# Performance work log

Hardware: AMD Instinct MI355X
Metric: run time of the kernel (lower is better)

## Reference

```python
import jax, jax.numpy as jnp
import numpy as np

B, T, D, H, V = 4096, 193, 50, 50, 11


def setup_inputs() -> dict:
    key = jax.random.key(0)
    ks = jax.random.split(key, 7)
    s = 1.0 / np.sqrt(H)
    return {
        "x": jax.random.normal(ks[0], (B, T, D), dtype=jnp.float32),
        "W_ih": jax.random.uniform(ks[1], (4 * H, D), jnp.float32, -s, s),
        "W_hh": jax.random.uniform(ks[2], (4 * H, H), jnp.float32, -s, s),
        "b_ih": jax.random.uniform(ks[3], (4 * H,), jnp.float32, -s, s),
        "b_hh": jax.random.uniform(ks[4], (4 * H,), jnp.float32, -s, s),
        "fc_w": jax.random.uniform(ks[5], (V, H), jnp.float32, -s, s),
        "fc_b": jax.random.uniform(ks[6], (V,), jnp.float32, -s, s),
    }


def _lstm_last_h(x, W_ih, W_hh, b_ih, b_hh):
    # Precompute input projections for all timesteps: [T, B, 4H]
    xp = jnp.einsum("btd,gd->tbg", x, W_ih) + (b_ih + b_hh)
    h0 = jnp.zeros((x.shape[0], H), x.dtype)
    c0 = jnp.zeros((x.shape[0], H), x.dtype)

    def step(carry, xt):
        h, c = carry
        gates = xt + h @ W_hh.T  # [B, 4H]
        i, f, g, o = jnp.split(gates, 4, axis=-1)  # PyTorch gate order i,f,g,o
        i = jax.nn.sigmoid(i)
        f = jax.nn.sigmoid(f)
        g = jnp.tanh(g)
        o = jax.nn.sigmoid(o)
        c = f * c + i * g
        h = o * jnp.tanh(c)
        return (h, c), None

    (h_last, _), _ = jax.lax.scan(step, (h0, c0), xp)
    return h_last


def reference(x, W_ih, W_hh, b_ih, b_hh, fc_w, fc_b):
    h = _lstm_last_h(x, W_ih, W_hh, b_ih, b_hh)  # [B, H]
    logits = jax.nn.relu(h) @ fc_w.T + fc_b       # [B, V]
    return jax.nn.log_softmax(logits, axis=-1)
```

## Files before the change

### kernel.cpp

```cpp
#include <hip/hip_runtime.h>
#include <math.h>

#define B_   4096
#define T_   193
#define D_   50
#define H_   50
#define V_   11
#define BT   16
#define NBLK (B_ / BT)
#define CH   16
#define NCH  ((T_ + CH - 1) / CH)
#define NTHREADS 448
#define NP   5

typedef __bf16 bf16x8 __attribute__((ext_vector_type(8)));
typedef float  f32x4  __attribute__((ext_vector_type(4)));

__device__ __forceinline__ float sigf(float v) { return 1.0f / (1.0f + __expf(-v)); }
__device__ __forceinline__ float thf(float v)  { return 2.0f / (1.0f + __expf(-2.0f * v)) - 1.0f; }

__device__ __forceinline__ void lgkm_barrier() {
    asm volatile("s_waitcnt lgkmcnt(0)\n\ts_barrier" ::: "memory");
}

__global__ __launch_bounds__(NTHREADS, 2) void lstm_mfma_kernel(
    const float* __restrict__ x,
    const float* __restrict__ W_ih,
    const float* __restrict__ W_hh,
    const float* __restrict__ b_ih,
    const float* __restrict__ b_hh,
    const float* __restrict__ fc_w,
    const float* __restrict__ fc_b,
    float* __restrict__ out)
{
    __shared__ __align__(16) unsigned short xs[2 * CH * 2 * 64 * 8];
    __shared__ __align__(16) unsigned short hb[2 * 4 * 64 * 8];
    __shared__ float hfin[BT * 53];
    __shared__ float lgts[BT][V_];

    const int tid  = threadIdx.x;
    const int wid  = tid >> 6;
    const int lane = tid & 63;
    const int n    = lane & 15;
    const int kg   = lane >> 4;
    const int row0 = blockIdx.x * BT;
    const int tA   = 2 * wid;
    const int tB   = 2 * wid + 1;

    {
        int4 z; z.x = 0; z.y = 0; z.z = 0; z.w = 0;
        #pragma unroll
        for (int i = tid; i < 512; i += NTHREADS)
            reinterpret_cast<int4*>(hb)[i] = z;
    }
    __syncthreads();
    if (tid < 32) {
        hb[(tid >> 4) * 2048 + 512 + (48 + (tid & 15)) * 8 + 7] = 0x3F80;
    }

    bf16x8 wxhA[2], wxlA[2], whhA[2], whlA[2];
    bf16x8 wxhB[2], wxlB[2], whhB[2], whlB[2];
    #pragma unroll
    for (int ti = 0; ti < 2; ++ti) {
        const int gp = 16 * (ti == 0 ? tA : tB) + n;
        const int q  = gp & 3;
        const int ju = gp >> 2;
        const bool real = (ju < 50);
        const int row = real ? (q * 50 + ju) : 0;
        #pragma unroll
        for (int s = 0; s < 2; ++s) {
            bf16x8 xh, xl, hh, hl;
            #pragma unroll
            for (int j = 0; j < 8; ++j) {
                const int k = s * 32 + kg * 8 + j;
                float vx = 0.0f, vh = 0.0f;
                if (real) {
                    if (k < 50) { vx = W_ih[row * 50 + k]; vh = W_hh[row * 50 + k]; }
                    if (k == 63) vh = b_ih[row] + b_hh[row];
                }
                const __bf16 xhi = (__bf16)vx;
                const __bf16 hhi = (__bf16)vh;
                xh[j] = xhi; xl[j] = (__bf16)(vx - (float)xhi);
                hh[j] = hhi; hl[j] = (__bf16)(vh - (float)hhi);
            }
            if (ti == 0) { wxhA[s] = xh; wxlA[s] = xl; whhA[s] = hh; whlA[s] = hl; }
            else         { wxhB[s] = xh; wxlB[s] = xl; whhB[s] = hh; whlB[s] = hl; }
        }
    }

    const int uA = 4 * tA + kg;
    const int uB = 4 * tB + kg;
    const int hoffA = (uA >> 5) * 512 + ((((uA & 31) >> 3) << 4) | n) * 8 + (uA & 7);
    const int hoffB = (uB >> 5) * 512 + ((((uB & 31) >> 3) << 4) | n) * 8 + (uB & 7);

    float2 P[NP][4];

    auto loadChunk = [&](int c) {
        const int t0 = c * CH;
        const int L  = (T_ - t0 < CH) ? (T_ - t0) : CH;
        const int nfrag = L * 128;
        #pragma unroll
        for (int i = 0; i < NP; ++i) {
            const int fi = tid + i * NTHREADS;
            if (fi < nfrag) {
                const int tc  = fi >> 7;
                const int rem = fi & 127;
                const int s   = rem >> 6;
                const int l   = rem & 63;
                const int nn  = l & 15;
                const int kk  = l >> 4;
                const float* base = x + ((size_t)(row0 + nn) * T_ + (t0 + tc)) * D_;
                #pragma unroll
                for (int j = 0; j < 4; ++j) {
                    int col = 32 * s + kk * 8 + 2 * j;
                    if (col > 48) col = 48;
                    P[i][j] = *reinterpret_cast<const float2*>(base + col);
                }
            }
        }
    };
    auto writeChunk = [&](int c, int b) {
        const int t0 = c * CH;
        const int L  = (T_ - t0 < CH) ? (T_ - t0) : CH;
        const int nfrag = L * 128;
        #pragma unroll
        for (int i = 0; i < NP; ++i) {
            const int fi = tid + i * NTHREADS;
            if (fi < nfrag) {
                bf16x8 w;
                #pragma unroll
                for (int j = 0; j < 4; ++j) {
                    w[2 * j]     = (__bf16)P[i][j].x;
                    w[2 * j + 1] = (__bf16)P[i][j].y;
                }
                reinterpret_cast<int4*>(xs)[b * (CH * 128) + fi] =
                    __builtin_bit_cast(int4, w);
            }
        }
    };

    loadChunk(0);
    writeChunk(0, 0);
    __syncthreads();
    loadChunk(1);

    float cstA = 0.0f, cstB = 0.0f;
    float hlastA = 0.0f, hlastB = 0.0f;
    const f32x4 zz = {0.0f, 0.0f, 0.0f, 0.0f};
    f32x4 axA, axB;
    const int4* xsv = reinterpret_cast<const int4*>(xs);
    const int4* hbv = reinterpret_cast<const int4*>(hb);

#define XPROJ(X0, X1)                                                         \
    {                                                                         \
        axA = __builtin_amdgcn_mfma_f32_16x16x32_bf16(wxhA[0], (X0), zz, 0, 0, 0);  \
        axA = __builtin_amdgcn_mfma_f32_16x16x32_bf16(wxhA[1], (X1), axA, 0, 0, 0); \
        axA = __builtin_amdgcn_mfma_f32_16x16x32_bf16(wxlA[0], (X0), axA, 0, 0, 0); \
        axA = __builtin_amdgcn_mfma_f32_16x16x32_bf16(wxlA[1], (X1), axA, 0, 0, 0); \
        axB = __builtin_amdgcn_mfma_f32_16x16x32_bf16(wxhB[0], (X0), zz, 0, 0, 0);  \
        axB = __builtin_amdgcn_mfma_f32_16x16x32_bf16(wxhB[1], (X1), axB, 0, 0, 0); \
        axB = __builtin_amdgcn_mfma_f32_16x16x32_bf16(wxlB[0], (X0), axB, 0, 0, 0); \
        axB = __builtin_amdgcn_mfma_f32_16x16x32_bf16(wxlB[1], (X1), axB, 0, 0, 0); \
    }

#define STEP(CUR, TC, LAST)                                                   \
    {                                                                         \
        const int4* hc = hbv + (CUR) * 256;                                   \
        const bf16x8 bh0 = __builtin_bit_cast(bf16x8, hc[lane]);              \
        const bf16x8 bh1 = __builtin_bit_cast(bf16x8, hc[64 + lane]);         \
        const bf16x8 bl0 = __builtin_bit_cast(bf16x8, hc[128 + lane]);        \
        const bf16x8 bl1 = __builtin_bit_cast(bf16x8, hc[192 + lane]);        \
        f32x4 aA = __builtin_amdgcn_mfma_f32_16x16x32_bf16(whhA[0], bh0, axA, 0, 0, 0); \
        aA = __builtin_amdgcn_mfma_f32_16x16x32_bf16(whhA[1], bh1, aA, 0, 0, 0);        \
        aA = __builtin_amdgcn_mfma_f32_16x16x32_bf16(whhA[0], bl0, aA, 0, 0, 0);        \
        aA = __builtin_amdgcn_mfma_f32_16x16x32_bf16(whhA[1], bl1, aA, 0, 0, 0);        \
        aA = __builtin_amdgcn_mfma_f32_16x16x32_bf16(whlA[0], bh0, aA, 0, 0, 0);        \
        aA = __builtin_amdgcn_mfma_f32_16x16x32_bf16(whlA[1], bh1, aA, 0, 0, 0);        \
        f32x4 aB = __builtin_amdgcn_mfma_f32_16x16x32_bf16(whhB[0], bh0, axB, 0, 0, 0); \
        aB = __builtin_amdgcn_mfma_f32_16x16x32_bf16(whhB[1], bh1, aB, 0, 0, 0);        \
        aB = __builtin_amdgcn_mfma_f32_16x16x32_bf16(whhB[0], bl0, aB, 0, 0, 0);        \
        aB = __builtin_amdgcn_mfma_f32_16x16x32_bf16(whhB[1], bl1, aB, 0, 0, 0);        \
        aB = __builtin_amdgcn_mfma_f32_16x16x32_bf16(whlB[0], bh0, aB, 0, 0, 0);        \
        aB = __builtin_amdgcn_mfma_f32_16x16x32_bf16(whlB[1], bh1, aB, 0, 0, 0);        \
        const float iiA = sigf(aA[0]);                                        \
        const float ffA = sigf(aA[1]);                                        \
        const float g2A = thf(aA[2]);                                         \
        const float ooA = sigf(aA[3]);                                        \
        cstA = fmaf(ffA, cstA, iiA * g2A);                                    \
        const float hA = ooA * thf(cstA);                                     \
        const float iiB = sigf(aB[0]);                                        \
        const float ffB = sigf(aB[1]);                                        \
        const float g2B = thf(aB[2]);                                         \
        const float ooB = sigf(aB[3]);                                        \
        cstB = fmaf(ffB, cstB, iiB * g2B);                                    \
        const float hB = ooB * thf(cstB);                                     \
        const __bf16 hAhi = (__bf16)hA;                                       \
        const __bf16 hBhi = (__bf16)hB;                                       \
        const __bf16 hAlo = (__bf16)(hA - (float)hAhi);                       \
        const __bf16 hBlo = (__bf16)(hB - (float)hBhi);                       \
        unsigned short* hw = hb + ((CUR) ^ 1) * 2048;                         \
        hw[hoffA]        = __builtin_bit_cast(unsigned short, hAhi);          \
        hw[hoffB]        = __builtin_bit_cast(unsigned short, hBhi);          \
        hw[1024 + hoffA] = __builtin_bit_cast(unsigned short, hAlo);          \
        hw[1024 + hoffB] = __builtin_bit_cast(unsigned short, hBlo);          \
        if (!(LAST)) {                                                        \
            const bf16x8 nx0 = __builtin_bit_cast(                            \
                bf16x8, xb[((TC) + 1) * 128 + lane]);                         \
            const bf16x8 nx1 = __builtin_bit_cast(                            \
                bf16x8, xb[((TC) + 1) * 128 + 64 + lane]);                    \
            XPROJ(nx0, nx1);                                                  \
        } else {                                                              \
            writeChunk(c + 1, bb ^ 1);                                        \
            if (c + 2 < NCH) loadChunk(c + 2);                                \
        }                                                                     \
        lgkm_barrier();                                                       \
    }

    for (int c = 0; c < NCH - 1; ++c) {
        const int bb = c & 1;
        const int4* xb = xsv + bb * (CH * 128);

        {
            const bf16x8 x0 = __builtin_bit_cast(bf16x8, xb[lane]);
            const bf16x8 x1 = __builtin_bit_cast(bf16x8, xb[64 + lane]);
            XPROJ(x0, x1);
        }
        #pragma unroll
        for (int p = 0; p < 8; ++p) {
            STEP(0, 2 * p, 0);
            STEP(1, 2 * p + 1, (2 * p + 1 == CH - 1));
        }
    }

    {
        const int4* xb = xsv;
        const bf16x8 x0 = __builtin_bit_cast(bf16x8, xb[lane]);
        const bf16x8 x1 = __builtin_bit_cast(bf16x8, xb[64 + lane]);
        XPROJ(x0, x1);

        const bf16x8 bh0 = __builtin_bit_cast(bf16x8, hbv[lane]);
        const bf16x8 bh1 = __builtin_bit_cast(bf16x8, hbv[64 + lane]);
        const bf16x8 bl0 = __builtin_bit_cast(bf16x8, hbv[128 + lane]);
        const bf16x8 bl1 = __builtin_bit_cast(bf16x8, hbv[192 + lane]);
        f32x4 aA = __builtin_amdgcn_mfma_f32_16x16x32_bf16(whhA[0], bh0, axA, 0, 0, 0);
        aA = __builtin_amdgcn_mfma_f32_16x16x32_bf16(whhA[1], bh1, aA, 0, 0, 0);
        aA = __builtin_amdgcn_mfma_f32_16x16x32_bf16(whhA[0], bl0, aA, 0, 0, 0);
        aA = __builtin_amdgcn_mfma_f32_16x16x32_bf16(whhA[1], bl1, aA, 0, 0, 0);
        aA = __builtin_amdgcn_mfma_f32_16x16x32_bf16(whlA[0], bh0, aA, 0, 0, 0);
        aA = __builtin_amdgcn_mfma_f32_16x16x32_bf16(whlA[1], bh1, aA, 0, 0, 0);
        f32x4 aB = __builtin_amdgcn_mfma_f32_16x16x32_bf16(whhB[0], bh0, axB, 0, 0, 0);
        aB = __builtin_amdgcn_mfma_f32_16x16x32_bf16(whhB[1], bh1, aB, 0, 0, 0);
        aB = __builtin_amdgcn_mfma_f32_16x16x32_bf16(whhB[0], bl0, aB, 0, 0, 0);
        aB = __builtin_amdgcn_mfma_f32_16x16x32_bf16(whhB[1], bl1, aB, 0, 0, 0);
        aB = __builtin_amdgcn_mfma_f32_16x16x32_bf16(whlB[0], bh0, aB, 0, 0, 0);
        aB = __builtin_amdgcn_mfma_f32_16x16x32_bf16(whlB[1], bh1, aB, 0, 0, 0);

        cstA = fmaf(sigf(aA[1]), cstA, sigf(aA[0]) * thf(aA[2]));
        hlastA = sigf(aA[3]) * thf(cstA);
        cstB = fmaf(sigf(aB[1]), cstB, sigf(aB[0]) * thf(aB[2]));
        hlastB = sigf(aB[3]) * thf(cstB);
    }

    if (uA < 50) hfin[n * 53 + uA] = hlastA;
    if (uB < 50) hfin[n * 53 + uB] = hlastB;
    __syncthreads();

    if (tid < BT * V_) {
        const int bn = tid / V_;
        const int v  = tid % V_;
        float a = fc_b[v];
        #pragma unroll
        for (int j = 0; j < 50; ++j) {
            float hj = hfin[bn * 53 + j];
            hj = hj > 0.0f ? hj : 0.0f;
            a = fmaf(hj, fc_w[v * 50 + j], a);
        }
        lgts[bn][v] = a;
    }
    __syncthreads();
    if (tid < BT * V_) {
        const int bn = tid / V_;
        const int v  = tid % V_;
        float m = -1e30f;
        #pragma unroll
        for (int u = 0; u < V_; ++u) m = fmaxf(m, lgts[bn][u]);
        float s = 0.0f;
        #pragma unroll
        for (int u = 0; u < V_; ++u) s += __expf(lgts[bn][u] - m);
        out[(size_t)(row0 + bn) * V_ + v] = lgts[bn][v] - m - __logf(s);
    }
}

extern "C" void kernel_launch(void* const* d_in, const int* in_sizes, int n_in,
                              void* d_out, int out_size, void* d_ws, size_t ws_size,
                              hipStream_t stream) {
    const float* x    = (const float*)d_in[0];
    const float* W_ih = (const float*)d_in[1];
    const float* W_hh = (const float*)d_in[2];
    const float* b_ih = (const float*)d_in[3];
    const float* b_hh = (const float*)d_in[4];
    const float* fc_w = (const float*)d_in[5];
    const float* fc_b = (const float*)d_in[6];
    float* out = (float*)d_out;

    lstm_mfma_kernel<<<NBLK, NTHREADS, 0, stream>>>(
        x, W_ih, W_hh, b_ih, b_hh, fc_w, fc_b, out);
}
```

Measured before the change: 214.3 us.

## Assign one gate tile per wave with 13 waves and split MFMA accumulation chains

Raises the block from 7 to 13 waves so each wave owns a single 16-row gate tile instead of two. This halves the per-wave serial MFMA and activation work on the recurrent critical path. The recurrent matmul is also split into two independent accumulator chains that are summed at the end, which shortens the MFMA dependency latency. In exchange, more waves must meet at the per-step barrier, and dropping the 2-blocks-per-CU launch bound may change occupancy.

```diff
diff --git a/kernel.cpp b/kernel.cpp
--- a/kernel.cpp
+++ b/kernel.cpp
@@ -10,8 +10,8 @@
 #define NBLK (B_ / BT)
 #define CH   16
 #define NCH  ((T_ + CH - 1) / CH)
-#define NTHREADS 448
-#define NP   5
+#define NTHREADS 832
+#define NP   3
 
 typedef __bf16 bf16x8 __attribute__((ext_vector_type(8)));
 typedef float  f32x4  __attribute__((ext_vector_type(4)));
@@ -23,7 +23,7 @@
     asm volatile("s_waitcnt lgkmcnt(0)\n\ts_barrier" ::: "memory");
 }
 
-__global__ __launch_bounds__(NTHREADS, 2) void lstm_mfma_kernel(
+__global__ __launch_bounds__(NTHREADS) void lstm_mfma_kernel(
     const float* __restrict__ x,
     const float* __restrict__ W_ih,
     const float* __restrict__ W_hh,
@@ -44,25 +44,20 @@
     const int n    = lane & 15;
     const int kg   = lane >> 4;
     const int row0 = blockIdx.x * BT;
-    const int tA   = 2 * wid;
-    const int tB   = 2 * wid + 1;
+    const int tile = wid;
 
     {
         int4 z; z.x = 0; z.y = 0; z.z = 0; z.w = 0;
-        #pragma unroll
-        for (int i = tid; i < 512; i += NTHREADS)
-            reinterpret_cast<int4*>(hb)[i] = z;
+        if (tid < 512) reinterpret_cast<int4*>(hb)[tid] = z;
     }
     __syncthreads();
     if (tid < 32) {
         hb[(tid >> 4) * 2048 + 512 + (48 + (tid & 15)) * 8 + 7] = 0x3F80;
     }
 
-    bf16x8 wxhA[2], wxlA[2], whhA[2], whlA[2];
-    bf16x8 wxhB[2], wxlB[2], whhB[2], whlB[2];
-    #pragma unroll
-    for (int ti = 0; ti < 2; ++ti) {
-        const int gp = 16 * (ti == 0 ? tA : tB) + n;
+    bf16x8 wxh[2], wxl[2], whh[2], whl[2];
+    {
+        const int gp = 16 * tile + n;
         const int q  = gp & 3;
         const int ju = gp >> 2;
         const bool real = (ju < 50);
@@ -83,15 +78,12 @@
                 xh[j] = xhi; xl[j] = (__bf16)(vx - (float)xhi);
                 hh[j] = hhi; hl[j] = (__bf16)(vh - (float)hhi);
             }
-            if (ti == 0) { wxhA[s] = xh; wxlA[s] = xl; whhA[s] = hh; whlA[s] = hl; }
-            else         { wxhB[s] = xh; wxlB[s] = xl; whhB[s] = hh; whlB[s] = hl; }
-        }
-    }
-
-    const int uA = 4 * tA + kg;
-    const int uB = 4 * tB + kg;
-    const int hoffA = (uA >> 5) * 512 + ((((uA & 31) >> 3) << 4) | n) * 8 + (uA & 7);
-    const int hoffB = (uB >> 5) * 512 + ((((uB & 31) >> 3) << 4) | n) * 8 + (uB & 7);
+            wxh[s] = xh; wxl[s] = xl; whh[s] = hh; whl[s] = hl;
+        }
+    }
+
+    const int u_   = 4 * tile + kg;
+    const int hoff = (u_ >> 5) * 512 + ((((u_ & 31) >> 3) << 4) | n) * 8 + (u_ & 7);
 
     float2 P[NP][4];
 
@@ -144,65 +136,47 @@
     __syncthreads();
     loadChunk(1);
 
-    float cstA = 0.0f, cstB = 0.0f;
-    float hlastA = 0.0f, hlastB = 0.0f;
+    float cst = 0.0f;
+    float hlast = 0.0f;
     const f32x4 zz = {0.0f, 0.0f, 0.0f, 0.0f};
-    f32x4 axA, axB;
+    f32x4 ax;
     const int4* xsv = reinterpret_cast<const int4*>(xs);
     const int4* hbv = reinterpret_cast<const int4*>(hb);
 
 #define XPROJ(X0, X1)                                                         \
     {                                                                         \
-        axA = __builtin_amdgcn_mfma_f32_16x16x32_bf16(wxhA[0], (X0), zz, 0, 0, 0);  \
-        axA = __builtin_amdgcn_mfma_f32_16x16x32_bf16(wxhA[1], (X1), axA, 0, 0, 0); \
-        axA = __builtin_amdgcn_mfma_f32_16x16x32_bf16(wxlA[0], (X0), axA, 0, 0, 0); \
-        axA = __builtin_amdgcn_mfma_f32_16x16x32_bf16(wxlA[1], (X1), axA, 0, 0, 0); \
-        axB = __builtin_amdgcn_mfma_f32_16x16x32_bf16(wxhB[0], (X0), zz, 0, 0, 0);  \
-        axB = __builtin_amdgcn_mfma_f32_16x16x32_bf16(wxhB[1], (X1), axB, 0, 0, 0); \
-        axB = __builtin_amdgcn_mfma_f32_16x16x32_bf16(wxlB[0], (X0), axB, 0, 0, 0); \
-        axB = __builtin_amdgcn_mfma_f32_16x16x32_bf16(wxlB[1], (X1), axB, 0, 0, 0); \
+        ax = __builtin_amdgcn_mfma_f32_16x16x32_bf16(wxh[0], (X0), zz, 0, 0, 0); \
+        ax = __builtin_amdgcn_mfma_f32_16x16x32_bf16(wxh[1], (X1), ax, 0, 0, 0); \
+        ax = __builtin_amdgcn_mfma_f32_16x16x32_bf16(wxl[0], (X0), ax, 0, 0, 0); \
+        ax = __builtin_amdgcn_mfma_f32_16x16x32_bf16(wxl[1], (X1), ax, 0, 0, 0); \
     }
 
 #define STEP(CUR, TC, LAST)                                                   \
     {                                                                         \
         const int4* hc = hbv + (CUR) * 256;                                   \
         const bf16x8 bh0 = __builtin_bit_cast(bf16x8, hc[lane]);              \
+        const bf16x8 bl0 = __builtin_bit_cast(bf16x8, hc[128 + lane]);        \
         const bf16x8 bh1 = __builtin_bit_cast(bf16x8, hc[64 + lane]);         \
-        const bf16x8 bl0 = __builtin_bit_cast(bf16x8, hc[128 + lane]);        \
         const bf16x8 bl1 = __builtin_bit_cast(bf16x8, hc[192 + lane]);        \
-        f32x4 aA = __builtin_amdgcn_mfma_f32_16x16x32_bf16(whhA[0], bh0, axA, 0, 0, 0); \
-        aA = __builtin_amdgcn_mfma_f32_16x16x32_bf16(whhA[1], bh1, aA, 0, 0, 0);        \
-        aA = __builtin_amdgcn_mfma_f32_16x16x32_bf16(whhA[0], bl0, aA, 0, 0, 0);        \
-        aA = __builtin_amdgcn_mfma_f32_16x16x32_bf16(whhA[1], bl1, aA, 0, 0, 0);        \
-        aA = __builtin_amdgcn_mfma_f32_16x16x32_bf16(whlA[0], bh0, aA, 0, 0, 0);        \
-        aA = __builtin_amdgcn_mfma_f32_16x16x32_bf16(whlA[1], bh1, aA, 0, 0, 0);        \
-        f32x4 aB = __builtin_amdgcn_mfma_f32_16x16x32_bf16(whhB[0], bh0, axB, 0, 0, 0); \
-        aB = __builtin_amdgcn_mfma_f32_16x16x32_bf16(whhB[1], bh1, aB, 0, 0, 0);        \
-        aB = __builtin_amdgcn_mfma_f32_16x16x32_bf16(whhB[0], bl0, aB, 0, 0, 0);        \
-        aB = __builtin_amdgcn_mfma_f32_16x16x32_bf16(whhB[1], bl1, aB, 0, 0, 0);        \
-        aB = __builtin_amdgcn_mfma_f32_16x16x32_bf16(whlB[0], bh0, aB, 0, 0, 0);        \
-        aB = __builtin_amdgcn_mfma_f32_16x16x32_bf16(whlB[1], bh1, aB, 0, 0, 0);        \
-        const float iiA = sigf(aA[0]);                                        \
-        const float ffA = sigf(aA[1]);                                        \
-        const float g2A = thf(aA[2]);                                         \
-        const float ooA = sigf(aA[3]);                                        \
-        cstA = fmaf(ffA, cstA, iiA * g2A);                                    \
-        const float hA = ooA * thf(cstA);                                     \
-        const float iiB = sigf(aB[0]);                                        \
-        const float ffB = sigf(aB[1]);                                        \
-        const float g2B = thf(aB[2]);                                         \
-        const float ooB = sigf(aB[3]);                                        \
-        cstB = fmaf(ffB, cstB, iiB * g2B);                                    \
-        const float hB = ooB * thf(cstB);                                     \
-        const __bf16 hAhi = (__bf16)hA;                                       \
-        const __bf16 hBhi = (__bf16)hB;                                       \
-        const __bf16 hAlo = (__bf16)(hA - (float)hAhi);                       \
-        const __bf16 hBlo = (__bf16)(hB - (float)hBhi);                       \
+        f32x4 c1 = __builtin_amdgcn_mfma_f32_16x16x32_bf16(whh[0], bh0, ax, 0, 0, 0); \
+        f32x4 c2 = __builtin_amdgcn_mfma_f32_16x16x32_bf16(whh[0], bl0, zz, 0, 0, 0); \
+        c1 = __builtin_amdgcn_mfma_f32_16x16x32_bf16(whh[1], bh1, c1, 0, 0, 0);       \
+        c2 = __builtin_amdgcn_mfma_f32_16x16x32_bf16(whh[1], bl1, c2, 0, 0, 0);       \
+        c1 = __builtin_amdgcn_mfma_f32_16x16x32_bf16(whl[0], bh0, c1, 0, 0, 0);       \
+        c2 = __builtin_amdgcn_mfma_f32_16x16x32_bf16(whl[1], bh1, c2, 0, 0, 0);       \
+        const f32x4 a = c1 + c2;                                              \
+        const float ii = sigf(a[0]);                                          \
+        const float ff = sigf(a[1]);                                          \
+        const float g2 = thf(a[2]);                                           \
+        const float oo = sigf(a[3]);                                          \
+        cst = fmaf(ff, cst, ii * g2);                                         \
+        const float h = oo * thf(cst);                                        \
+        hlast = h;                                                            \
+        const __bf16 hhi = (__bf16)h;                                         \
+        const __bf16 hlo = (__bf16)(h - (float)hhi);                          \
         unsigned short* hw = hb + ((CUR) ^ 1) * 2048;                         \
-        hw[hoffA]        = __builtin_bit_cast(unsigned short, hAhi);          \
-        hw[hoffB]        = __builtin_bit_cast(unsigned short, hBhi);          \
-        hw[1024 + hoffA] = __builtin_bit_cast(unsigned short, hAlo);          \
-        hw[1024 + hoffB] = __builtin_bit_cast(unsigned short, hBlo);          \
+        hw[hoff]        = __builtin_bit_cast(unsigned short, hhi);            \
+        hw[1024 + hoff] = __builtin_bit_cast(unsigned short, hlo);            \
         if (!(LAST)) {                                                        \
             const bf16x8 nx0 = __builtin_bit_cast(                            \
                 bf16x8, xb[((TC) + 1) * 128 + lane]);                         \
@@ -239,30 +213,22 @@
         XPROJ(x0, x1);
 
         const bf16x8 bh0 = __builtin_bit_cast(bf16x8, hbv[lane]);
+        const bf16x8 bl0 = __builtin_bit_cast(bf16x8, hbv[128 + lane]);
         const bf16x8 bh1 = __builtin_bit_cast(bf16x8, hbv[64 + lane]);
-        const bf16x8 bl0 = __builtin_bit_cast(bf16x8, hbv[128 + lane]);
         const bf16x8 bl1 = __builtin_bit_cast(bf16x8, hbv[192 + lane]);
-        f32x4 aA = __builtin_amdgcn_mfma_f32_16x16x32_bf16(whhA[0], bh0, axA, 0, 0, 0);
-        aA = __builtin_amdgcn_mfma_f32_16x16x32_bf16(whhA[1], bh1, aA, 0, 0, 0);
-        aA = __builtin_amdgcn_mfma_f32_16x16x32_bf16(whhA[0], bl0, aA, 0, 0, 0);
-        aA = __builtin_amdgcn_mfma_f32_16x16x32_bf16(whhA[1], bl1, aA, 0, 0, 0);
-        aA = __builtin_amdgcn_mfma_f32_16x16x32_bf16(whlA[0], bh0, aA, 0, 0, 0);
-        aA = __builtin_amdgcn_mfma_f32_16x16x32_bf16(whlA[1], bh1, aA, 0, 0, 0);
-        f32x4 aB = __builtin_amdgcn_mfma_f32_16x16x32_bf16(whhB[0], bh0, axB, 0, 0, 0);
-        aB = __builtin_amdgcn_mfma_f32_16x16x32_bf16(whhB[1], bh1, aB, 0, 0, 0);
-        aB = __builtin_amdgcn_mfma_f32_16x16x32_bf16(whhB[0], bl0, aB, 0, 0, 0);
-        aB = __builtin_amdgcn_mfma_f32_16x16x32_bf16(whhB[1], bl1, aB, 0, 0, 0);
-        aB = __builtin_amdgcn_mfma_f32_16x16x32_bf16(whlB[0], bh0, aB, 0, 0, 0);
-        aB = __builtin_amdgcn_mfma_f32_16x16x32_bf16(whlB[1], bh1, aB, 0, 0, 0);
-
-        cstA = fmaf(sigf(aA[1]), cstA, sigf(aA[0]) * thf(aA[2]));
-        hlastA = sigf(aA[3]) * thf(cstA);
-        cstB = fmaf(sigf(aB[1]), cstB, sigf(aB[0]) * thf(aB[2]));
-        hlastB = sigf(aB[3]) * thf(cstB);
-    }
-
-    if (uA < 50) hfin[n * 53 + uA] = hlastA;
-    if (uB < 50) hfin[n * 53 + uB] = hlastB;
+        f32x4 c1 = __builtin_amdgcn_mfma_f32_16x16x32_bf16(whh[0], bh0, ax, 0, 0, 0);
+        f32x4 c2 = __builtin_amdgcn_mfma_f32_16x16x32_bf16(whh[0], bl0, zz, 0, 0, 0);
+        c1 = __builtin_amdgcn_mfma_f32_16x16x32_bf16(whh[1], bh1, c1, 0, 0, 0);
+        c2 = __builtin_amdgcn_mfma_f32_16x16x32_bf16(whh[1], bl1, c2, 0, 0, 0);
+        c1 = __builtin_amdgcn_mfma_f32_16x16x32_bf16(whl[0], bh0, c1, 0, 0, 0);
+        c2 = __builtin_amdgcn_mfma_f32_16x16x32_bf16(whl[1], bh1, c2, 0, 0, 0);
+        const f32x4 a = c1 + c2;
+
+        cst = fmaf(sigf(a[1]), cst, sigf(a[0]) * thf(a[2]));
+        hlast = sigf(a[3]) * thf(cst);
+    }
+
+    if (u_ < 50) hfin[n * 53 + u_] = hlast;
     __syncthreads();
 
     if (tid < BT * V_) {
```

New measurement: 218.4 us. Within noise of the previous version (+1.9%).
